# Kernel optimization log

Measured on AMD Instinct MI355X. Metric: run time of the kernel, lower is better.

The kernel has to match this reference:

```python
import jax, jax.numpy as jnp
import numpy as np

N_SPEAKERS = 65536
HIDDEN = 1024
EMBED = 1024
DIM_UPDATE = 2048
LN_EPS = 1e-5


def setup_inputs() -> dict:
    key = jax.random.key(0)
    ks = jax.random.split(key, 8)
    s = 0.02
    return {
        "u_t": jax.random.normal(ks[0], (EMBED,), dtype=jnp.float32),
        "speaker_embeddings": jax.random.normal(ks[1], (N_SPEAKERS, HIDDEN), dtype=jnp.float32),
        "W_attn": jax.random.normal(ks[2], (HIDDEN, EMBED), dtype=jnp.float32) * s,
        "W1": jax.random.normal(ks[3], (DIM_UPDATE, HIDDEN + 2 * EMBED), dtype=jnp.float32) * s,
        "b1": jnp.zeros((DIM_UPDATE,), dtype=jnp.float32),
        "W2": jax.random.normal(ks[4], (HIDDEN, DIM_UPDATE), dtype=jnp.float32) * s,
        "b2": jnp.zeros((HIDDEN,), dtype=jnp.float32),
        "ln_gamma": jnp.ones((HIDDEN,), dtype=jnp.float32),
        "ln_beta": jnp.zeros((HIDDEN,), dtype=jnp.float32),
        "s_i": 12345,
    }


def reference(u_t, speaker_embeddings, W_attn, W1, b1, W2, b2, ln_gamma, ln_beta, s_i):
    # query = attention_projection(u_t): Linear(embed->hidden, bias=False) -> [HIDDEN]
    query = W_attn @ u_t
    # attention over the whole speaker memory bank: [N]
    attn_weights = jax.nn.softmax(speaker_embeddings @ query, axis=0)
    # weighted sum of bank rows: [HIDDEN]
    context = attn_weights @ speaker_embeddings
    h_s = speaker_embeddings[s_i]  # [HIDDEN]
    update_material = jnp.concatenate([u_t, h_s, context], axis=-1)  # [HIDDEN+2*EMBED]
    # update_gate: Linear -> GELU -> (dropout=id) -> Linear -> (dropout=id) -> LayerNorm
    h = jax.nn.gelu(update_material @ W1.T + b1, approximate=False)
    o = h @ W2.T + b2
    mu = jnp.mean(o)
    var = jnp.mean(jnp.square(o - mu))
    new_h_s = (o - mu) * jax.lax.rsqrt(var + LN_EPS) * ln_gamma + ln_beta
    # clone + indexed scatter write of the residual-updated row
    new_embeddings = speaker_embeddings.at[s_i].set(h_s + new_h_s)
    return new_embeddings
```

## Files before the change

kernel.cpp:

```cpp
#include <hip/hip_runtime.h>
#include <math.h>

#define NSPK  65536
#define HID   1024
#define DUP   2048
#define CAT   3072
#define LN_EPS 1e-5f

typedef float f4 __attribute__((ext_vector_type(4)));

constexpr int K1_NBLK = 1024;
constexpr int K2_NBLK = 64;

#define WS_QUERY   0
#define WS_CONTEXT 1024
#define WS_H       2048
#define WS_O       4096
#define WS_PM      5120
#define WS_PL      (WS_PM + K1_NBLK)
#define WS_PC      8192

__device__ __forceinline__ float wave_sum64(float d) {
#pragma unroll
  for (int s = 32; s > 0; s >>= 1) d += __shfl_xor(d, s, 64);
  return d;
}

__global__ __launch_bounds__(256) void k0_query(
    const float* __restrict__ W_attn, const float* __restrict__ u_t,
    float* __restrict__ query) {
  const int lane = threadIdx.x & 63;
  const int wv = threadIdx.x >> 6;
  const int row = blockIdx.x * 4 + wv;
  const float* rp = W_attn + (size_t)row * HID;
  float d = 0.f;
#pragma unroll
  for (int i = 0; i < 4; ++i) {
    f4 v = *(const f4*)(rp + i * 256 + lane * 4);
    f4 u = *(const f4*)(u_t + i * 256 + lane * 4);
    f4 p = v * u;
    d += p.x + p.y + p.z + p.w;
  }
  d = wave_sum64(d);
  if (lane == 0) query[row] = d;
}

__global__ __launch_bounds__(256) void k1_pass(
    const float* __restrict__ emb, const float* __restrict__ query,
    float* __restrict__ out, float* __restrict__ pm, float* __restrict__ pl,
    float* __restrict__ pc) {
  const int tid = threadIdx.x;
  const int lane = tid & 63;
  const int wv = tid >> 6;
  const int gw = blockIdx.x * 4 + wv;
  const int col = lane * 4;

  f4 q0 = *(const f4*)(query + 0 * 256 + col);
  f4 q1 = *(const f4*)(query + 1 * 256 + col);
  f4 q2 = *(const f4*)(query + 2 * 256 + col);
  f4 q3 = *(const f4*)(query + 3 * 256 + col);

  float m = -INFINITY, l = 0.f;
  f4 c0 = {0.f, 0.f, 0.f, 0.f}, c1 = c0, c2 = c0, c3 = c0;

  const int row0 = gw * 16;
  const float* rp0 = emb + (size_t)row0 * HID + col;
  f4 v0 = __builtin_nontemporal_load((const f4*)(rp0 + 0 * 256));
  f4 v1 = __builtin_nontemporal_load((const f4*)(rp0 + 1 * 256));
  f4 v2 = __builtin_nontemporal_load((const f4*)(rp0 + 2 * 256));
  f4 v3 = __builtin_nontemporal_load((const f4*)(rp0 + 3 * 256));

  for (int r = 0; r < 16; ++r) {
    f4 n0, n1, n2, n3;
    if (r < 15) {
      const float* np = emb + (size_t)(row0 + r + 1) * HID + col;
      n0 = __builtin_nontemporal_load((const f4*)(np + 0 * 256));
      n1 = __builtin_nontemporal_load((const f4*)(np + 1 * 256));
      n2 = __builtin_nontemporal_load((const f4*)(np + 2 * 256));
      n3 = __builtin_nontemporal_load((const f4*)(np + 3 * 256));
    } else {
      n0 = v0; n1 = v1; n2 = v2; n3 = v3;
    }
    float* op = out + (size_t)(row0 + r) * HID + col;
    __builtin_nontemporal_store(v0, (f4*)(op + 0 * 256));
    __builtin_nontemporal_store(v1, (f4*)(op + 1 * 256));
    __builtin_nontemporal_store(v2, (f4*)(op + 2 * 256));
    __builtin_nontemporal_store(v3, (f4*)(op + 3 * 256));
    f4 p = v0 * q0 + v1 * q1 + v2 * q2 + v3 * q3;
    float d = p.x + p.y + p.z + p.w;
    d = wave_sum64(d);
    if (d > m + 8.f) {
      float alpha = __expf(m - d);
      l *= alpha;
      c0 *= alpha; c1 *= alpha; c2 *= alpha; c3 *= alpha;
      m = d;
    }
    float w = __expf(d - m);
    l += w;
    c0 += w * v0; c1 += w * v1; c2 += w * v2; c3 += w * v3;
    v0 = n0; v1 = n1; v2 = n2; v3 = n3;
  }

  __shared__ float sm[4], sl[4];
  __shared__ f4 sc[4][256];
  if (lane == 0) { sm[wv] = m; sl[wv] = l; }
  sc[wv][0 * 64 + lane] = c0;
  sc[wv][1 * 64 + lane] = c1;
  sc[wv][2 * 64 + lane] = c2;
  sc[wv][3 * 64 + lane] = c3;
  __syncthreads();

  const float M = fmaxf(fmaxf(sm[0], sm[1]), fmaxf(sm[2], sm[3]));
  const float w0 = __expf(sm[0] - M), w1 = __expf(sm[1] - M);
  const float w2 = __expf(sm[2] - M), w3 = __expf(sm[3] - M);

  f4 a = w0 * sc[0][tid] + w1 * sc[1][tid] + w2 * sc[2][tid] + w3 * sc[3][tid];
  ((f4*)(pc + (size_t)blockIdx.x * HID))[tid] = a;
  if (tid == 0) {
    pm[blockIdx.x] = M;
    pl[blockIdx.x] = w0 * sl[0] + w1 * sl[1] + w2 * sl[2] + w3 * sl[3];
  }
}

__global__ __launch_bounds__(256) void k2_reduce(
    const float* __restrict__ pm, const float* __restrict__ pl,
    const float* __restrict__ pc, float* __restrict__ context) {
  __shared__ float red[256];
  __shared__ float sw[K1_NBLK];
  const int tid = threadIdx.x;

  float mx = -INFINITY;
  for (int p = tid; p < K1_NBLK; p += 256) mx = fmaxf(mx, pm[p]);
  red[tid] = mx;
  __syncthreads();
  for (int s = 128; s > 0; s >>= 1) {
    if (tid < s) red[tid] = fmaxf(red[tid], red[tid + s]);
    __syncthreads();
  }
  const float M = red[0];
  __syncthreads();

  float ls = 0.f;
  for (int p = tid; p < K1_NBLK; p += 256) {
    float w = __expf(pm[p] - M);
    sw[p] = w;
    ls += w * pl[p];
  }
  red[tid] = ls;
  __syncthreads();
  for (int s = 128; s > 0; s >>= 1) {
    if (tid < s) red[tid] += red[tid + s];
    __syncthreads();
  }
  const float invL = 1.f / red[0];

  const int ci = tid & 15;
  const int p0 = tid >> 4;
  const int c = blockIdx.x * 16 + ci;
  float acc = 0.f;
#pragma unroll 4
  for (int p = p0; p < K1_NBLK; p += 16)
    acc += sw[p] * pc[(size_t)p * HID + c];

  __shared__ float sacc[256];
  sacc[tid] = acc;
  __syncthreads();
  for (int s = 128; s >= 16; s >>= 1) {
    if (tid < s) sacc[tid] += sacc[tid + s];
    __syncthreads();
  }
  if (tid < 16) context[blockIdx.x * 16 + tid] = sacc[tid] * invL;
}

__global__ __launch_bounds__(256) void k3_fc1(
    const float* __restrict__ W1, const float* __restrict__ b1,
    const float* __restrict__ u_t, const float* __restrict__ emb,
    const int* __restrict__ s_i_p, const float* __restrict__ context,
    float* __restrict__ h) {
  const int lane = threadIdx.x & 63;
  const int wv = threadIdx.x >> 6;
  const int row = blockIdx.x * 4 + wv;
  const float* rp = W1 + (size_t)row * CAT;
  const int s_i = *s_i_p;
  const float* hs = emb + (size_t)s_i * HID;
  float d = 0.f;
#pragma unroll
  for (int i = 0; i < 12; ++i) {
    const int k = i * 256 + lane * 4;
    f4 v = *(const f4*)(rp + k);
    const float* src = (i < 4) ? (u_t + k) : (i < 8) ? (hs + k - 1024)
                                                     : (context + k - 2048);
    f4 u = *(const f4*)src;
    f4 p = v * u;
    d += p.x + p.y + p.z + p.w;
  }
  d = wave_sum64(d);
  if (lane == 0) {
    float x = d + b1[row];
    h[row] = 0.5f * x * (1.0f + erff(x * 0.70710678118654752f));
  }
}

__global__ __launch_bounds__(256) void k4_fc2(
    const float* __restrict__ W2, const float* __restrict__ b2,
    const float* __restrict__ h, float* __restrict__ o) {
  const int lane = threadIdx.x & 63;
  const int wv = threadIdx.x >> 6;
  const int row = blockIdx.x * 4 + wv;
  const float* rp = W2 + (size_t)row * DUP;
  float d = 0.f;
#pragma unroll
  for (int i = 0; i < 8; ++i) {
    const int k = i * 256 + lane * 4;
    f4 v = *(const f4*)(rp + k);
    f4 u = *(const f4*)(h + k);
    f4 p = v * u;
    d += p.x + p.y + p.z + p.w;
  }
  d = wave_sum64(d);
  if (lane == 0) o[row] = d + b2[row];
}

__global__ __launch_bounds__(256) void k5_ln_scatter(
    const float* __restrict__ o, const float* __restrict__ gamma,
    const float* __restrict__ beta, const float* __restrict__ emb,
    const int* __restrict__ s_i_p, float* __restrict__ out) {
  __shared__ float red[256];
  const int tid = threadIdx.x;
  f4 v = *(const f4*)(o + tid * 4);
  float s = v.x + v.y + v.z + v.w;
  red[tid] = s;
  __syncthreads();
  for (int t = 128; t > 0; t >>= 1) {
    if (tid < t) red[tid] += red[tid + t];
    __syncthreads();
  }
  const float mu = red[0] * (1.0f / HID);
  __syncthreads();
  float dx = v.x - mu, dy = v.y - mu, dz = v.z - mu, dw = v.w - mu;
  red[tid] = dx * dx + dy * dy + dz * dz + dw * dw;
  __syncthreads();
  for (int t = 128; t > 0; t >>= 1) {
    if (tid < t) red[tid] += red[tid + t];
    __syncthreads();
  }
  const float var = red[0] * (1.0f / HID);
  const float inv = rsqrtf(var + LN_EPS);
  const int s_i = *s_i_p;
  const float* hs = emb + (size_t)s_i * HID;
  f4 g = *(const f4*)(gamma + tid * 4);
  f4 b = *(const f4*)(beta + tid * 4);
  f4 hv = *(const f4*)(hs + tid * 4);
  f4 r;
  r.x = hv.x + dx * inv * g.x + b.x;
  r.y = hv.y + dy * inv * g.y + b.y;
  r.z = hv.z + dz * inv * g.z + b.z;
  r.w = hv.w + dw * inv * g.w + b.w;
  *(f4*)(out + (size_t)s_i * HID + tid * 4) = r;
}

extern "C" void kernel_launch(void* const* d_in, const int* in_sizes, int n_in,
                              void* d_out, int out_size, void* d_ws, size_t ws_size,
                              hipStream_t stream) {
  const float* u_t     = (const float*)d_in[0];
  const float* emb     = (const float*)d_in[1];
  const float* W_attn  = (const float*)d_in[2];
  const float* W1      = (const float*)d_in[3];
  const float* b1      = (const float*)d_in[4];
  const float* W2      = (const float*)d_in[5];
  const float* b2      = (const float*)d_in[6];
  const float* gamma   = (const float*)d_in[7];
  const float* beta    = (const float*)d_in[8];
  const int*   s_i_p   = (const int*)d_in[9];
  float* out = (float*)d_out;

  float* ws = (float*)d_ws;
  float* query   = ws + WS_QUERY;
  float* context = ws + WS_CONTEXT;
  float* h       = ws + WS_H;
  float* o       = ws + WS_O;
  float* pm      = ws + WS_PM;
  float* pl      = ws + WS_PL;
  float* pc      = ws + WS_PC;

  k0_query<<<256, 256, 0, stream>>>(W_attn, u_t, query);
  k1_pass<<<K1_NBLK, 256, 0, stream>>>(emb, query, out, pm, pl, pc);
  k2_reduce<<<K2_NBLK, 256, 0, stream>>>(pm, pl, pc, context);
  k3_fc1<<<512, 256, 0, stream>>>(W1, b1, u_t, emb, s_i_p, context, h);
  k4_fc2<<<256, 256, 0, stream>>>(W2, b2, h, o);
  k5_ln_scatter<<<1, 256, 0, stream>>>(o, gamma, beta, emb, s_i_p, out);
}
```

Baseline: 495.2 us.

## Fuse attention pass, reduction, MLP and LayerNorm into one persistent kernel with grid barriers

Replaces five separate launches (streaming pass, partial reduction, fc1, fc2, LN scatter) with one persistent kernel of 256 blocks of 1024 threads. The stages are separated by atomic-counter grid barriers, and the counter is reset in the query kernel. This removes launch gaps and tail effects between the small dependent stages, and the streaming pass now uses 256 larger blocks instead of 1024. The risk is lower memory-level parallelism in the bandwidth-bound pass, plus a deadlock if all 256 blocks are not co-resident.

```diff
diff --git a/kernel.cpp b/kernel.cpp
--- a/kernel.cpp
+++ b/kernel.cpp
@@ -9,15 +9,15 @@
 
 typedef float f4 __attribute__((ext_vector_type(4)));
 
-constexpr int K1_NBLK = 1024;
-constexpr int K2_NBLK = 64;
+constexpr int NB = 256;
 
 #define WS_QUERY   0
 #define WS_CONTEXT 1024
 #define WS_H       2048
 #define WS_O       4096
 #define WS_PM      5120
-#define WS_PL      (WS_PM + K1_NBLK)
+#define WS_PL      5376
+#define WS_CNT     5632
 #define WS_PC      8192
 
 __device__ __forceinline__ float wave_sum64(float d) {
@@ -25,10 +25,32 @@
   for (int s = 32; s > 0; s >>= 1) d += __shfl_xor(d, s, 64);
   return d;
 }
-
-__global__ __launch_bounds__(256) void k0_query(
+__device__ __forceinline__ float wave_max64(float d) {
+#pragma unroll
+  for (int s = 32; s > 0; s >>= 1) d = fmaxf(d, __shfl_xor(d, s, 64));
+  return d;
+}
+
+__device__ __forceinline__ void gbar_arrive(int* cnt) {
+  __syncthreads();
+  if (threadIdx.x == 0) {
+    __threadfence();
+    atomicAdd(cnt, 1);
+  }
+}
+__device__ __forceinline__ void gbar_wait(int* cnt, int target) {
+  if (threadIdx.x == 0) {
+    while (__hip_atomic_load(cnt, __ATOMIC_ACQUIRE, __HIP_MEMORY_SCOPE_AGENT) < target)
+      __builtin_amdgcn_s_sleep(2);
+    __threadfence();
+  }
+  __syncthreads();
+}
+
+__global__ __launch_bounds__(256) void kA_query(
     const float* __restrict__ W_attn, const float* __restrict__ u_t,
-    float* __restrict__ query) {
+    float* __restrict__ query, int* __restrict__ cnt) {
+  if (blockIdx.x == 0 && threadIdx.x == 0) *cnt = 0;
   const int lane = threadIdx.x & 63;
   const int wv = threadIdx.x >> 6;
   const int row = blockIdx.x * 4 + wv;
@@ -45,236 +67,13 @@
   if (lane == 0) query[row] = d;
 }
 
-__global__ __launch_bounds__(256) void k1_pass(
-    const float* __restrict__ emb, const float* __restrict__ query,
-    float* __restrict__ out, float* __restrict__ pm, float* __restrict__ pl,
-    float* __restrict__ pc) {
-  const int tid = threadIdx.x;
-  const int lane = tid & 63;
-  const int wv = tid >> 6;
-  const int gw = blockIdx.x * 4 + wv;
-  const int col = lane * 4;
-
-  f4 q0 = *(const f4*)(query + 0 * 256 + col);
-  f4 q1 = *(const f4*)(query + 1 * 256 + col);
-  f4 q2 = *(const f4*)(query + 2 * 256 + col);
-  f4 q3 = *(const f4*)(query + 3 * 256 + col);
-
-  float m = -INFINITY, l = 0.f;
-  f4 c0 = {0.f, 0.f, 0.f, 0.f}, c1 = c0, c2 = c0, c3 = c0;
-
-  const int row0 = gw * 16;
-  const float* rp0 = emb + (size_t)row0 * HID + col;
-  f4 v0 = __builtin_nontemporal_load((const f4*)(rp0 + 0 * 256));
-  f4 v1 = __builtin_nontemporal_load((const f4*)(rp0 + 1 * 256));
-  f4 v2 = __builtin_nontemporal_load((const f4*)(rp0 + 2 * 256));
-  f4 v3 = __builtin_nontemporal_load((const f4*)(rp0 + 3 * 256));
-
-  for (int r = 0; r < 16; ++r) {
-    f4 n0, n1, n2, n3;
-    if (r < 15) {
-      const float* np = emb + (size_t)(row0 + r + 1) * HID + col;
-      n0 = __builtin_nontemporal_load((const f4*)(np + 0 * 256));
-      n1 = __builtin_nontemporal_load((const f4*)(np + 1 * 256));
-      n2 = __builtin_nontemporal_load((const f4*)(np + 2 * 256));
-      n3 = __builtin_nontemporal_load((const f4*)(np + 3 * 256));
-    } else {
-      n0 = v0; n1 = v1; n2 = v2; n3 = v3;
-    }
-    float* op = out + (size_t)(row0 + r) * HID + col;
-    __builtin_nontemporal_store(v0, (f4*)(op + 0 * 256));
-    __builtin_nontemporal_store(v1, (f4*)(op + 1 * 256));
-    __builtin_nontemporal_store(v2, (f4*)(op + 2 * 256));
-    __builtin_nontemporal_store(v3, (f4*)(op + 3 * 256));
-    f4 p = v0 * q0 + v1 * q1 + v2 * q2 + v3 * q3;
-    float d = p.x + p.y + p.z + p.w;
-    d = wave_sum64(d);
-    if (d > m + 8.f) {
-      float alpha = __expf(m - d);
-      l *= alpha;
-      c0 *= alpha; c1 *= alpha; c2 *= alpha; c3 *= alpha;
-      m = d;
-    }
-    float w = __expf(d - m);
-    l += w;
-    c0 += w * v0; c1 += w * v1; c2 += w * v2; c3 += w * v3;
-    v0 = n0; v1 = n1; v2 = n2; v3 = n3;
-  }
-
-  __shared__ float sm[4], sl[4];
-  __shared__ f4 sc[4][256];
-  if (lane == 0) { sm[wv] = m; sl[wv] = l; }
-  sc[wv][0 * 64 + lane] = c0;
-  sc[wv][1 * 64 + lane] = c1;
-  sc[wv][2 * 64 + lane] = c2;
-  sc[wv][3 * 64 + lane] = c3;
-  __syncthreads();
-
-  const float M = fmaxf(fmaxf(sm[0], sm[1]), fmaxf(sm[2], sm[3]));
-  const float w0 = __expf(sm[0] - M), w1 = __expf(sm[1] - M);
-  const float w2 = __expf(sm[2] - M), w3 = __expf(sm[3] - M);
-
-  f4 a = w0 * sc[0][tid] + w1 * sc[1][tid] + w2 * sc[2][tid] + w3 * sc[3][tid];
-  ((f4*)(pc + (size_t)blockIdx.x * HID))[tid] = a;
-  if (tid == 0) {
-    pm[blockIdx.x] = M;
-    pl[blockIdx.x] = w0 * sl[0] + w1 * sl[1] + w2 * sl[2] + w3 * sl[3];
-  }
-}
-
-__global__ __launch_bounds__(256) void k2_reduce(
-    const float* __restrict__ pm, const float* __restrict__ pl,
-    const float* __restrict__ pc, float* __restrict__ context) {
-  __shared__ float red[256];
-  __shared__ float sw[K1_NBLK];
-  const int tid = threadIdx.x;
-
-  float mx = -INFINITY;
-  for (int p = tid; p < K1_NBLK; p += 256) mx = fmaxf(mx, pm[p]);
-  red[tid] = mx;
-  __syncthreads();
-  for (int s = 128; s > 0; s >>= 1) {
-    if (tid < s) red[tid] = fmaxf(red[tid], red[tid + s]);
-    __syncthreads();
-  }
-  const float M = red[0];
-  __syncthreads();
-
-  float ls = 0.f;
-  for (int p = tid; p < K1_NBLK; p += 256) {
-    float w = __expf(pm[p] - M);
-    sw[p] = w;
-    ls += w * pl[p];
-  }
-  red[tid] = ls;
-  __syncthreads();
-  for (int s = 128; s > 0; s >>= 1) {
-    if (tid < s) red[tid] += red[tid + s];
-    __syncthreads();
-  }
-  const float invL = 1.f / red[0];
-
-  const int ci = tid & 15;
-  const int p0 = tid >> 4;
-  const int c = blockIdx.x * 16 + ci;
-  float acc = 0.f;
-#pragma unroll 4
-  for (int p = p0; p < K1_NBLK; p += 16)
-    acc += sw[p] * pc[(size_t)p * HID + c];
-
-  __shared__ float sacc[256];
-  sacc[tid] = acc;
-  __syncthreads();
-  for (int s = 128; s >= 16; s >>= 1) {
-    if (tid < s) sacc[tid] += sacc[tid + s];
-    __syncthreads();
-  }
-  if (tid < 16) context[blockIdx.x * 16 + tid] = sacc[tid] * invL;
-}
-
-__global__ __launch_bounds__(256) void k3_fc1(
+__global__ __launch_bounds__(1024, 4) void kB_fused(
+    const float* __restrict__ u_t, const float* __restrict__ emb,
     const float* __restrict__ W1, const float* __restrict__ b1,
-    const float* __restrict__ u_t, const float* __restrict__ emb,
-    const int* __restrict__ s_i_p, const float* __restrict__ context,
-    float* __restrict__ h) {
-  const int lane = threadIdx.x & 63;
-  const int wv = threadIdx.x >> 6;
-  const int row = blockIdx.x * 4 + wv;
-  const float* rp = W1 + (size_t)row * CAT;
-  const int s_i = *s_i_p;
-  const float* hs = emb + (size_t)s_i * HID;
-  float d = 0.f;
-#pragma unroll
-  for (int i = 0; i < 12; ++i) {
-    const int k = i * 256 + lane * 4;
-    f4 v = *(const f4*)(rp + k);
-    const float* src = (i < 4) ? (u_t + k) : (i < 8) ? (hs + k - 1024)
-                                                     : (context + k - 2048);
-    f4 u = *(const f4*)src;
-    f4 p = v * u;
-    d += p.x + p.y + p.z + p.w;
-  }
-  d = wave_sum64(d);
-  if (lane == 0) {
-    float x = d + b1[row];
-    h[row] = 0.5f * x * (1.0f + erff(x * 0.70710678118654752f));
-  }
-}
-
-__global__ __launch_bounds__(256) void k4_fc2(
     const float* __restrict__ W2, const float* __restrict__ b2,
-    const float* __restrict__ h, float* __restrict__ o) {
-  const int lane = threadIdx.x & 63;
-  const int wv = threadIdx.x >> 6;
-  const int row = blockIdx.x * 4 + wv;
-  const float* rp = W2 + (size_t)row * DUP;
-  float d = 0.f;
-#pragma unroll
-  for (int i = 0; i < 8; ++i) {
-    const int k = i * 256 + lane * 4;
-    f4 v = *(const f4*)(rp + k);
-    f4 u = *(const f4*)(h + k);
-    f4 p = v * u;
-    d += p.x + p.y + p.z + p.w;
-  }
-  d = wave_sum64(d);
-  if (lane == 0) o[row] = d + b2[row];
-}
-
-__global__ __launch_bounds__(256) void k5_ln_scatter(
-    const float* __restrict__ o, const float* __restrict__ gamma,
-    const float* __restrict__ beta, const float* __restrict__ emb,
-    const int* __restrict__ s_i_p, float* __restrict__ out) {
-  __shared__ float red[256];
-  const int tid = threadIdx.x;
-  f4 v = *(const f4*)(o + tid * 4);
-  float s = v.x + v.y + v.z + v.w;
-  red[tid] = s;
-  __syncthreads();
-  for (int t = 128; t > 0; t >>= 1) {
-    if (tid < t) red[tid] += red[tid + t];
-    __syncthreads();
-  }
-  const float mu = red[0] * (1.0f / HID);
-  __syncthreads();
-  float dx = v.x - mu, dy = v.y - mu, dz = v.z - mu, dw = v.w - mu;
-  red[tid] = dx * dx + dy * dy + dz * dz + dw * dw;
-  __syncthreads();
-  for (int t = 128; t > 0; t >>= 1) {
-    if (tid < t) red[tid] += red[tid + t];
-    __syncthreads();
-  }
-  const float var = red[0] * (1.0f / HID);
-  const float inv = rsqrtf(var + LN_EPS);
-  const int s_i = *s_i_p;
-  const float* hs = emb + (size_t)s_i * HID;
-  f4 g = *(const f4*)(gamma + tid * 4);
-  f4 b = *(const f4*)(beta + tid * 4);
-  f4 hv = *(const f4*)(hs + tid * 4);
-  f4 r;
-  r.x = hv.x + dx * inv * g.x + b.x;
-  r.y = hv.y + dy * inv * g.y + b.y;
-  r.z = hv.z + dz * inv * g.z + b.z;
-  r.w = hv.w + dw * inv * g.w + b.w;
-  *(f4*)(out + (size_t)s_i * HID + tid * 4) = r;
-}
-
-extern "C" void kernel_launch(void* const* d_in, const int* in_sizes, int n_in,
-                              void* d_out, int out_size, void* d_ws, size_t ws_size,
-                              hipStream_t stream) {
-  const float* u_t     = (const float*)d_in[0];
-  const float* emb     = (const float*)d_in[1];
-  const float* W_attn  = (const float*)d_in[2];
-  const float* W1      = (const float*)d_in[3];
-  const float* b1      = (const float*)d_in[4];
-  const float* W2      = (const float*)d_in[5];
-  const float* b2      = (const float*)d_in[6];
-  const float* gamma   = (const float*)d_in[7];
-  const float* beta    = (const float*)d_in[8];
-  const int*   s_i_p   = (const int*)d_in[9];
-  float* out = (float*)d_out;
-
-  float* ws = (float*)d_ws;
+    const float* __restrict__ gamma, const float* __restrict__ beta,
+    const int* __restrict__ s_i_p, float* __restrict__ out,
+    float* __restrict__ ws) {
   float* query   = ws + WS_QUERY;
   float* context = ws + WS_CONTEXT;
   float* h       = ws + WS_H;
@@ -282,11 +81,226 @@
   float* pm      = ws + WS_PM;
   float* pl      = ws + WS_PL;
   float* pc      = ws + WS_PC;
-
-  k0_query<<<256, 256, 0, stream>>>(W_attn, u_t, query);
-  k1_pass<<<K1_NBLK, 256, 0, stream>>>(emb, query, out, pm, pl, pc);
-  k2_reduce<<<K2_NBLK, 256, 0, stream>>>(pm, pl, pc, context);
-  k3_fc1<<<512, 256, 0, stream>>>(W1, b1, u_t, emb, s_i_p, context, h);
-  k4_fc2<<<256, 256, 0, stream>>>(W2, b2, h, o);
-  k5_ln_scatter<<<1, 256, 0, stream>>>(o, gamma, beta, emb, s_i_p, out);
-}
+  int*   cnt     = (int*)(ws + WS_CNT);
+
+  const int tid  = threadIdx.x;
+  const int lane = tid & 63;
+  const int wv   = tid >> 6;
+  const int bid  = blockIdx.x;
+
+  __shared__ float sm[16], sl[16], sh[16], sred[16];
+  __shared__ f4 sc[16][256];
+  __shared__ float sw[256];
+  __shared__ float sacc[1024];
+
+  {
+    const int gw = bid * 16 + wv;
+    const int col = lane * 4;
+    f4 q0 = *(const f4*)(query + 0 * 256 + col);
+    f4 q1 = *(const f4*)(query + 1 * 256 + col);
+    f4 q2 = *(const f4*)(query + 2 * 256 + col);
+    f4 q3 = *(const f4*)(query + 3 * 256 + col);
+
+    float m = -INFINITY, l = 0.f;
+    f4 c0 = {0.f, 0.f, 0.f, 0.f}, c1 = c0, c2 = c0, c3 = c0;
+
+    const int row0 = gw * 16;
+    const float* rp0 = emb + (size_t)row0 * HID + col;
+    f4 v0 = __builtin_nontemporal_load((const f4*)(rp0 + 0 * 256));
+    f4 v1 = __builtin_nontemporal_load((const f4*)(rp0 + 1 * 256));
+    f4 v2 = __builtin_nontemporal_load((const f4*)(rp0 + 2 * 256));
+    f4 v3 = __builtin_nontemporal_load((const f4*)(rp0 + 3 * 256));
+
+    for (int r = 0; r < 16; ++r) {
+      f4 n0, n1, n2, n3;
+      if (r < 15) {
+        const float* np = emb + (size_t)(row0 + r + 1) * HID + col;
+        n0 = __builtin_nontemporal_load((const f4*)(np + 0 * 256));
+        n1 = __builtin_nontemporal_load((const f4*)(np + 1 * 256));
+        n2 = __builtin_nontemporal_load((const f4*)(np + 2 * 256));
+        n3 = __builtin_nontemporal_load((const f4*)(np + 3 * 256));
+      } else {
+        n0 = v0; n1 = v1; n2 = v2; n3 = v3;
+      }
+      float* op = out + (size_t)(row0 + r) * HID + col;
+      __builtin_nontemporal_store(v0, (f4*)(op + 0 * 256));
+      __builtin_nontemporal_store(v1, (f4*)(op + 1 * 256));
+      __builtin_nontemporal_store(v2, (f4*)(op + 2 * 256));
+      __builtin_nontemporal_store(v3, (f4*)(op + 3 * 256));
+      f4 p = v0 * q0 + v1 * q1 + v2 * q2 + v3 * q3;
+      float d = p.x + p.y + p.z + p.w;
+      d = wave_sum64(d);
+      if (d > m + 8.f) {
+        float alpha = __expf(m - d);
+        l *= alpha;
+        c0 *= alpha; c1 *= alpha; c2 *= alpha; c3 *= alpha;
+        m = d;
+      }
+      float w = __expf(d - m);
+      l += w;
+      c0 += w * v0; c1 += w * v1; c2 += w * v2; c3 += w * v3;
+      v0 = n0; v1 = n1; v2 = n2; v3 = n3;
+    }
+
+    if (lane == 0) { sm[wv] = m; sl[wv] = l; }
+    sc[wv][0 * 64 + lane] = c0;
+    sc[wv][1 * 64 + lane] = c1;
+    sc[wv][2 * 64 + lane] = c2;
+    sc[wv][3 * 64 + lane] = c3;
+    __syncthreads();
+
+    float M = sm[0];
+#pragma unroll
+    for (int i = 1; i < 16; ++i) M = fmaxf(M, sm[i]);
+    if (tid < 256) {
+      float wgt[16];
+#pragma unroll
+      for (int i = 0; i < 16; ++i) wgt[i] = __expf(sm[i] - M);
+      f4 a = {0.f, 0.f, 0.f, 0.f};
+#pragma unroll
+      for (int i = 0; i < 16; ++i) a += wgt[i] * sc[i][tid];
+      ((f4*)(pc + (size_t)bid * HID))[tid] = a;
+      if (tid == 0) {
+        float L = 0.f;
+#pragma unroll
+        for (int i = 0; i < 16; ++i) L += wgt[i] * sl[i];
+        pm[bid] = M;
+        pl[bid] = L;
+      }
+    }
+  }
+  gbar_arrive(cnt);
+  gbar_wait(cnt, NB);
+
+  {
+    float mi = (tid < NB) ? pm[tid] : -INFINITY;
+    float mw = wave_max64(mi);
+    if (lane == 0) sred[wv] = mw;
+    __syncthreads();
+    float M = sred[0];
+#pragma unroll
+    for (int i = 1; i < 16; ++i) M = fmaxf(M, sred[i]);
+
+    float li = 0.f;
+    if (tid < NB) {
+      float w = __expf(pm[tid] - M);
+      sw[tid] = w;
+      li = w * pl[tid];
+    }
+    float lw = wave_sum64(li);
+    __syncthreads();
+    if (lane == 0) sred[wv] = lw;
+    __syncthreads();
+    float L = 0.f;
+#pragma unroll
+    for (int i = 0; i < 16; ++i) L += sred[i];
+    const float invL = 1.f / L;
+
+    const int c = bid * 4 + (tid & 3);
+    const int p = tid >> 2;
+    sacc[tid] = sw[p] * pc[(size_t)p * HID + c];
+    __syncthreads();
+    for (int s = 512; s >= 4; s >>= 1) {
+      if (tid < s) sacc[tid] += sacc[tid + s];
+      __syncthreads();
+    }
+    if (tid < 4) context[bid * 4 + tid] = sacc[tid] * invL;
+  }
+  gbar_arrive(cnt);
+  gbar_wait(cnt, 2 * NB);
+
+  {
+    const int row = bid * 8 + (wv >> 1);
+    const int half = wv & 1;
+    const float* rp = W1 + (size_t)row * CAT;
+    const int s_i = *s_i_p;
+    const float* hs = emb + (size_t)s_i * HID;
+    float d = 0.f;
+#pragma unroll
+    for (int j = 0; j < 6; ++j) {
+      const int i = half * 6 + j;
+      const int k = i * 256 + lane * 4;
+      f4 v = *(const f4*)(rp + k);
+      const float* src = (i < 4) ? (u_t + k) : (i < 8) ? (hs + k - 1024)
+                                                       : (context + k - 2048);
+      f4 u = *(const f4*)src;
+      f4 p = v * u;
+      d += p.x + p.y + p.z + p.w;
+    }
+    d = wave_sum64(d);
+    if (lane == 0) sh[wv] = d;
+    __syncthreads();
+    if (half == 0 && lane == 0) {
+      float x = sh[wv] + sh[wv + 1] + b1[row];
+      h[row] = 0.5f * x * (1.0f + erff(x * 0.70710678118654752f));
+    }
+  }
+  gbar_arrive(cnt);
+  gbar_wait(cnt, 3 * NB);
+
+  {
+    const int row = bid * 4 + (wv >> 2);
+    const int q = wv & 3;
+    const float* rp = W2 + (size_t)row * DUP;
+    const int k0 = q * 512 + lane * 4;
+    f4 v0 = *(const f4*)(rp + k0);
+    f4 u0 = *(const f4*)(h + k0);
+    f4 v1 = *(const f4*)(rp + k0 + 256);
+    f4 u1 = *(const f4*)(h + k0 + 256);
+    f4 p = v0 * u0 + v1 * u1;
+    float d = wave_sum64(p.x + p.y + p.z + p.w);
+    if (lane == 0) sh[wv] = d;
+    __syncthreads();
+    if (q == 0 && lane == 0)
+      o[row] = sh[wv] + sh[wv + 1] + sh[wv + 2] + sh[wv + 3] + b2[row];
+  }
+  gbar_arrive(cnt);
+  if (bid != 0) return;
+  gbar_wait(cnt, 4 * NB);
+
+  {
+    float v = o[tid];
+    float s = wave_sum64(v);
+    if (lane == 0) sred[wv] = s;
+    __syncthreads();
+    float mu = 0.f;
+#pragma unroll
+    for (int i = 0; i < 16; ++i) mu += sred[i];
+    mu *= (1.0f / HID);
+    float dv = v - mu;
+    float q2 = wave_sum64(dv * dv);
+    __syncthreads();
+    if (lane == 0) sred[wv] = q2;
+    __syncthreads();
+    float var = 0.f;
+#pragma unroll
+    for (int i = 0; i < 16; ++i) var += sred[i];
+    var *= (1.0f / HID);
+    const float inv = rsqrtf(var + LN_EPS);
+    const int s_i = *s_i_p;
+    out[(size_t)s_i * HID + tid] =
+        emb[(size_t)s_i * HID + tid] + dv * inv * gamma[tid] + beta[tid];
+  }
+}
+
+extern "C" void kernel_launch(void* const* d_in, const int* in_sizes, int n_in,
+                              void* d_out, int out_size, void* d_ws, size_t ws_size,
+                              hipStream_t stream) {
+  const float* u_t    = (const float*)d_in[0];
+  const float* emb    = (const float*)d_in[1];
+  const float* W_attn = (const float*)d_in[2];
+  const float* W1     = (const float*)d_in[3];
+  const float* b1     = (const float*)d_in[4];
+  const float* W2     = (const float*)d_in[5];
+  const float* b2     = (const float*)d_in[6];
+  const float* gamma  = (const float*)d_in[7];
+  const float* beta   = (const float*)d_in[8];
+  const int*   s_i_p  = (const int*)d_in[9];
+  float* out = (float*)d_out;
+  float* ws  = (float*)d_ws;
+
+  kA_query<<<256, 256, 0, stream>>>(W_attn, u_t, ws + WS_QUERY,
+                                    (int*)(ws + WS_CNT));
+  kB_fused<<<NB, 1024, 0, stream>>>(u_t, emb, W1, b1, W2, b2, gamma, beta,
+                                    s_i_p, out, ws);
+}
```

Measured after the change: 550.8 us. 1.11x slower.

## Widen parallelism across attention pass, reduction, and both MLP GEMVs

Applied to the files above, without the earlier changes.

The streaming attention pass now uses 512-thread blocks with 8 rows per wave, so twice as many waves each do a shorter row chain. The cross-block reduction uses 1024 threads with wave-level max/sum shuffles instead of shared-memory tree loops. Both fc1 and fc2 split each output row across two waves and combine the halves through shared memory, doubling the grid. The goal is more latency hiding and memory-level parallelism on the bandwidth-bound passes, at the cost of shorter per-wave pipelining and extra shared-memory combines.

```diff
diff --git a/kernel.cpp b/kernel.cpp
--- a/kernel.cpp
+++ b/kernel.cpp
@@ -10,19 +10,23 @@
 typedef float f4 __attribute__((ext_vector_type(4)));
 
 constexpr int K1_NBLK = 1024;
-constexpr int K2_NBLK = 64;
 
 #define WS_QUERY   0
 #define WS_CONTEXT 1024
 #define WS_H       2048
 #define WS_O       4096
 #define WS_PM      5120
-#define WS_PL      (WS_PM + K1_NBLK)
+#define WS_PL      6144
 #define WS_PC      8192
 
 __device__ __forceinline__ float wave_sum64(float d) {
 #pragma unroll
   for (int s = 32; s > 0; s >>= 1) d += __shfl_xor(d, s, 64);
+  return d;
+}
+__device__ __forceinline__ float wave_max64(float d) {
+#pragma unroll
+  for (int s = 32; s > 0; s >>= 1) d = fmaxf(d, __shfl_xor(d, s, 64));
   return d;
 }
 
@@ -45,14 +49,14 @@
   if (lane == 0) query[row] = d;
 }
 
-__global__ __launch_bounds__(256) void k1_pass(
+__global__ __launch_bounds__(512) void k1_pass(
     const float* __restrict__ emb, const float* __restrict__ query,
     float* __restrict__ out, float* __restrict__ pm, float* __restrict__ pl,
     float* __restrict__ pc) {
   const int tid = threadIdx.x;
   const int lane = tid & 63;
   const int wv = tid >> 6;
-  const int gw = blockIdx.x * 4 + wv;
+  const int gw = blockIdx.x * 8 + wv;
   const int col = lane * 4;
 
   f4 q0 = *(const f4*)(query + 0 * 256 + col);
@@ -63,16 +67,16 @@
   float m = -INFINITY, l = 0.f;
   f4 c0 = {0.f, 0.f, 0.f, 0.f}, c1 = c0, c2 = c0, c3 = c0;
 
-  const int row0 = gw * 16;
+  const int row0 = gw * 8;
   const float* rp0 = emb + (size_t)row0 * HID + col;
   f4 v0 = __builtin_nontemporal_load((const f4*)(rp0 + 0 * 256));
   f4 v1 = __builtin_nontemporal_load((const f4*)(rp0 + 1 * 256));
   f4 v2 = __builtin_nontemporal_load((const f4*)(rp0 + 2 * 256));
   f4 v3 = __builtin_nontemporal_load((const f4*)(rp0 + 3 * 256));
 
-  for (int r = 0; r < 16; ++r) {
+  for (int r = 0; r < 8; ++r) {
     f4 n0, n1, n2, n3;
-    if (r < 15) {
+    if (r < 7) {
       const float* np = emb + (size_t)(row0 + r + 1) * HID + col;
       n0 = __builtin_nontemporal_load((const f4*)(np + 0 * 256));
       n1 = __builtin_nontemporal_load((const f4*)(np + 1 * 256));
@@ -101,8 +105,8 @@
     v0 = n0; v1 = n1; v2 = n2; v3 = n3;
   }
 
-  __shared__ float sm[4], sl[4];
-  __shared__ f4 sc[4][256];
+  __shared__ float sm[8], sl[8];
+  __shared__ f4 sc[8][256];
   if (lane == 0) { sm[wv] = m; sl[wv] = l; }
   sc[wv][0 * 64 + lane] = c0;
   sc[wv][1 * 64 + lane] = c1;
@@ -110,63 +114,65 @@
   sc[wv][3 * 64 + lane] = c3;
   __syncthreads();
 
-  const float M = fmaxf(fmaxf(sm[0], sm[1]), fmaxf(sm[2], sm[3]));
-  const float w0 = __expf(sm[0] - M), w1 = __expf(sm[1] - M);
-  const float w2 = __expf(sm[2] - M), w3 = __expf(sm[3] - M);
-
-  f4 a = w0 * sc[0][tid] + w1 * sc[1][tid] + w2 * sc[2][tid] + w3 * sc[3][tid];
-  ((f4*)(pc + (size_t)blockIdx.x * HID))[tid] = a;
-  if (tid == 0) {
-    pm[blockIdx.x] = M;
-    pl[blockIdx.x] = w0 * sl[0] + w1 * sl[1] + w2 * sl[2] + w3 * sl[3];
-  }
-}
-
-__global__ __launch_bounds__(256) void k2_reduce(
+  if (tid < 256) {
+    float M = sm[0];
+#pragma unroll
+    for (int i = 1; i < 8; ++i) M = fmaxf(M, sm[i]);
+    float wgt[8];
+#pragma unroll
+    for (int i = 0; i < 8; ++i) wgt[i] = __expf(sm[i] - M);
+    f4 a = {0.f, 0.f, 0.f, 0.f};
+#pragma unroll
+    for (int i = 0; i < 8; ++i) a += wgt[i] * sc[i][tid];
+    ((f4*)(pc + (size_t)blockIdx.x * HID))[tid] = a;
+    if (tid == 0) {
+      float L = 0.f;
+#pragma unroll
+      for (int i = 0; i < 8; ++i) L += wgt[i] * sl[i];
+      pm[blockIdx.x] = M;
+      pl[blockIdx.x] = L;
+    }
+  }
+}
+
+__global__ __launch_bounds__(1024) void k2_reduce(
     const float* __restrict__ pm, const float* __restrict__ pl,
     const float* __restrict__ pc, float* __restrict__ context) {
-  __shared__ float red[256];
+  __shared__ float sred[16];
   __shared__ float sw[K1_NBLK];
+  __shared__ float sacc[1024];
   const int tid = threadIdx.x;
-
-  float mx = -INFINITY;
-  for (int p = tid; p < K1_NBLK; p += 256) mx = fmaxf(mx, pm[p]);
-  red[tid] = mx;
-  __syncthreads();
-  for (int s = 128; s > 0; s >>= 1) {
-    if (tid < s) red[tid] = fmaxf(red[tid], red[tid + s]);
-    __syncthreads();
-  }
-  const float M = red[0];
-  __syncthreads();
-
-  float ls = 0.f;
-  for (int p = tid; p < K1_NBLK; p += 256) {
-    float w = __expf(pm[p] - M);
-    sw[p] = w;
-    ls += w * pl[p];
-  }
-  red[tid] = ls;
-  __syncthreads();
-  for (int s = 128; s > 0; s >>= 1) {
-    if (tid < s) red[tid] += red[tid + s];
-    __syncthreads();
-  }
-  const float invL = 1.f / red[0];
+  const int lane = tid & 63;
+  const int wvi = tid >> 6;
+
+  float mx = wave_max64(pm[tid]);
+  if (lane == 0) sred[wvi] = mx;
+  __syncthreads();
+  float M = sred[0];
+#pragma unroll
+  for (int i = 1; i < 16; ++i) M = fmaxf(M, sred[i]);
+
+  float w = __expf(pm[tid] - M);
+  sw[tid] = w;
+  float ls = wave_sum64(w * pl[tid]);
+  __syncthreads();
+  if (lane == 0) sred[wvi] = ls;
+  __syncthreads();
+  float L = 0.f;
+#pragma unroll
+  for (int i = 0; i < 16; ++i) L += sred[i];
+  const float invL = 1.f / L;
 
   const int ci = tid & 15;
   const int p0 = tid >> 4;
   const int c = blockIdx.x * 16 + ci;
   float acc = 0.f;
 #pragma unroll 4
-  for (int p = p0; p < K1_NBLK; p += 16)
-    acc += sw[p] * pc[(size_t)p * HID + c];
-
-  __shared__ float sacc[256];
+  for (int p = p0; p < K1_NBLK; p += 64) acc += sw[p] * pc[(size_t)p * HID + c];
   sacc[tid] = acc;
   __syncthreads();
-  for (int s = 128; s >= 16; s >>= 1) {
-    if (tid < s) sacc[tid] += sacc[tid + s];
+  for (int s = 32; s >= 1; s >>= 1) {
+    if ((tid >> 4) < s) sacc[tid] += sacc[tid + s * 16];
     __syncthreads();
   }
   if (tid < 16) context[blockIdx.x * 16 + tid] = sacc[tid] * invL;
@@ -177,15 +183,18 @@
     const float* __restrict__ u_t, const float* __restrict__ emb,
     const int* __restrict__ s_i_p, const float* __restrict__ context,
     float* __restrict__ h) {
+  __shared__ float sh[4];
   const int lane = threadIdx.x & 63;
   const int wv = threadIdx.x >> 6;
-  const int row = blockIdx.x * 4 + wv;
+  const int row = blockIdx.x * 2 + (wv >> 1);
+  const int half = wv & 1;
   const float* rp = W1 + (size_t)row * CAT;
   const int s_i = *s_i_p;
   const float* hs = emb + (size_t)s_i * HID;
   float d = 0.f;
 #pragma unroll
-  for (int i = 0; i < 12; ++i) {
+  for (int j = 0; j < 6; ++j) {
+    const int i = half * 6 + j;
     const int k = i * 256 + lane * 4;
     f4 v = *(const f4*)(rp + k);
     const float* src = (i < 4) ? (u_t + k) : (i < 8) ? (hs + k - 1024)
@@ -195,8 +204,10 @@
     d += p.x + p.y + p.z + p.w;
   }
   d = wave_sum64(d);
-  if (lane == 0) {
-    float x = d + b1[row];
+  if (lane == 0) sh[wv] = d;
+  __syncthreads();
+  if (half == 0 && lane == 0) {
+    float x = sh[wv] + sh[wv + 1] + b1[row];
     h[row] = 0.5f * x * (1.0f + erff(x * 0.70710678118654752f));
   }
 }
@@ -204,21 +215,26 @@
 __global__ __launch_bounds__(256) void k4_fc2(
     const float* __restrict__ W2, const float* __restrict__ b2,
     const float* __restrict__ h, float* __restrict__ o) {
+  __shared__ float sh[4];
   const int lane = threadIdx.x & 63;
   const int wv = threadIdx.x >> 6;
-  const int row = blockIdx.x * 4 + wv;
+  const int row = blockIdx.x * 2 + (wv >> 1);
+  const int half = wv & 1;
   const float* rp = W2 + (size_t)row * DUP;
-  float d = 0.f;
-#pragma unroll
-  for (int i = 0; i < 8; ++i) {
-    const int k = i * 256 + lane * 4;
-    f4 v = *(const f4*)(rp + k);
-    f4 u = *(const f4*)(h + k);
-    f4 p = v * u;
-    d += p.x + p.y + p.z + p.w;
-  }
-  d = wave_sum64(d);
-  if (lane == 0) o[row] = d + b2[row];
+  const int k0 = half * 1024 + lane * 4;
+  f4 v0 = *(const f4*)(rp + k0);
+  f4 u0 = *(const f4*)(h + k0);
+  f4 v1 = *(const f4*)(rp + k0 + 256);
+  f4 u1 = *(const f4*)(h + k0 + 256);
+  f4 v2 = *(const f4*)(rp + k0 + 512);
+  f4 u2 = *(const f4*)(h + k0 + 512);
+  f4 v3 = *(const f4*)(rp + k0 + 768);
+  f4 u3 = *(const f4*)(h + k0 + 768);
+  f4 p = v0 * u0 + v1 * u1 + v2 * u2 + v3 * u3;
+  float d = wave_sum64(p.x + p.y + p.z + p.w);
+  if (lane == 0) sh[wv] = d;
+  __syncthreads();
+  if (half == 0 && lane == 0) o[row] = sh[wv] + sh[wv + 1] + b2[row];
 }
 
 __global__ __launch_bounds__(256) void k5_ln_scatter(
@@ -262,16 +278,16 @@
 extern "C" void kernel_launch(void* const* d_in, const int* in_sizes, int n_in,
                               void* d_out, int out_size, void* d_ws, size_t ws_size,
                               hipStream_t stream) {
-  const float* u_t     = (const float*)d_in[0];
-  const float* emb     = (const float*)d_in[1];
-  const float* W_attn  = (const float*)d_in[2];
-  const float* W1      = (const float*)d_in[3];
-  const float* b1      = (const float*)d_in[4];
-  const float* W2      = (const float*)d_in[5];
-  const float* b2      = (const float*)d_in[6];
-  const float* gamma   = (const float*)d_in[7];
-  const float* beta    = (const float*)d_in[8];
-  const int*   s_i_p   = (const int*)d_in[9];
+  const float* u_t    = (const float*)d_in[0];
+  const float* emb    = (const float*)d_in[1];
+  const float* W_attn = (const float*)d_in[2];
+  const float* W1     = (const float*)d_in[3];
+  const float* b1     = (const float*)d_in[4];
+  const float* W2     = (const float*)d_in[5];
+  const float* b2     = (const float*)d_in[6];
+  const float* gamma  = (const float*)d_in[7];
+  const float* beta   = (const float*)d_in[8];
+  const int*   s_i_p  = (const int*)d_in[9];
   float* out = (float*)d_out;
 
   float* ws = (float*)d_ws;
@@ -284,9 +300,9 @@
   float* pc      = ws + WS_PC;
 
   k0_query<<<256, 256, 0, stream>>>(W_attn, u_t, query);
-  k1_pass<<<K1_NBLK, 256, 0, stream>>>(emb, query, out, pm, pl, pc);
-  k2_reduce<<<K2_NBLK, 256, 0, stream>>>(pm, pl, pc, context);
-  k3_fc1<<<512, 256, 0, stream>>>(W1, b1, u_t, emb, s_i_p, context, h);
-  k4_fc2<<<256, 256, 0, stream>>>(W2, b2, h, o);
+  k1_pass<<<K1_NBLK, 512, 0, stream>>>(emb, query, out, pm, pl, pc);
+  k2_reduce<<<64, 1024, 0, stream>>>(pm, pl, pc, context);
+  k3_fc1<<<1024, 256, 0, stream>>>(W1, b1, u_t, emb, s_i_p, context, h);
+  k4_fc2<<<512, 256, 0, stream>>>(W2, b2, h, o);
   k5_ln_scatter<<<1, 256, 0, stream>>>(o, gamma, beta, emb, s_i_p, out);
 }
```

Result: faster. 477.8 us (-3.5%).
